# Kernel tuning notes

Measured on AMD Instinct MI355X. Metric: run time of the kernel, lower is better.

Reference implementation:

```python
import jax, jax.numpy as jnp
import numpy as np

NUM_JOINTS = 50
FEAT = 3 * NUM_JOINTS  # 150

def _skeleton_bones():
    # Standard 50-joint sign-language skeleton (body + two 21-joint hands).
    body = [(0, 1), (1, 2), (2, 3), (3, 4), (1, 5), (5, 6), (6, 7)]
    def hand(conn_from, wrist):
        bones = [(conn_from, wrist)]
        for f in range(5):  # 5 fingers, chains of 4 joints from the wrist
            base = wrist + 1 + 4 * f
            bones.append((wrist, base))
            for k in range(3):
                bones.append((base + k, base + k + 1))
        return bones
    bones = body + hand(7, 8) + hand(4, 29)  # 49 bones
    bones.append((0, 2))  # pad to 50 bones so 3*num_bones == 150 matches the mask
    return np.asarray(bones, dtype=np.int32)

_BONES = _skeleton_bones()
_BA = jnp.asarray(_BONES[:, 0])  # (50,) bone endpoint a
_BB = jnp.asarray(_BONES[:, 1])  # (50,) bone endpoint b

def get_length_direct(x):
    # x: (B, T, 150) -> lengths (B, T, 50), directs (B, T, 150)
    B, T, _ = x.shape
    joints = x.reshape(B, T, NUM_JOINTS, 3)
    diff = joints[:, :, _BA, :] - joints[:, :, _BB, :]  # (B, T, 50, 3)
    length = jnp.sqrt(jnp.sum(diff * diff, axis=-1, keepdims=True))  # (B, T, 50, 1)
    tiny = jnp.finfo(x.dtype).tiny
    direct = diff / (length + tiny)  # unit directions
    return length[..., 0], direct.reshape(B, T, -1)

def setup_inputs() -> dict:
    key = jax.random.key(0)
    k1, k2 = jax.random.split(key)
    B, T = 64, 4096
    preds = jax.random.normal(k1, (B, T, FEAT), dtype=jnp.float32)
    targets = jax.random.normal(k2, (B, T, FEAT), dtype=jnp.float32)
    return {"preds": preds, "targets": targets}

def reference(preds, targets):
    target_pad = 0.0
    m = (targets != target_pad).astype(preds.dtype)  # (B, T, 150)
    pm = preds * m
    tm = targets * m
    _, pd = get_length_direct(pm)   # (B, T, 150)
    _, td = get_length_direct(tm)
    pd = pd * m  # mask[:, :, :150] == full mask since 3*num_bones == 150
    td = td * m
    # criterion = L1 (mean), criterion_bone = MSE (mean)
    recon = jnp.mean(jnp.abs(pm - tm)) + 0.1 * jnp.mean((pd - td) ** 2)
    return recon
```

## Files before the change

kernel.cpp:

```cpp
#include <hip/hip_runtime.h>
#include <stdint.h>

#define NUM_BONES  50
#define FEAT       150
#define FPT        8
#define THREADS    256
#define TILE_FLOATS (FPT * FEAT)
#define TOTAL_FRAMES (64 * 4096)
#define TOTAL_TILES  (TOTAL_FRAMES / FPT)
#define GRID_BLOCKS  2048
#define TILES_PER_BLOCK (TOTAL_TILES / GRID_BLOCKS)
#define NTASK      (FPT * NUM_BONES)

__device__ __constant__ int c_ba[NUM_BONES] = {
    0, 1, 2, 3, 1, 5, 6,
    7, 8, 9, 10, 11, 8, 13, 14, 15, 8, 17, 18, 19,
    8, 21, 22, 23, 8, 25, 26, 27,
    4, 29, 30, 31, 32, 29, 34, 35, 36, 29, 38, 39, 40,
    29, 42, 43, 44, 29, 46, 47, 48,
    0
};
__device__ __constant__ int c_bb[NUM_BONES] = {
    1, 2, 3, 4, 5, 6, 7,
    8, 9, 10, 11, 12, 13, 14, 15, 16, 17, 18, 19, 20,
    21, 22, 23, 24, 25, 26, 27, 28,
    29, 30, 31, 32, 33, 34, 35, 36, 37, 38, 39, 40, 41,
    42, 43, 44, 45, 46, 47, 48, 49,
    2
};

#define AS1 __attribute__((address_space(1)))
#define AS3 __attribute__((address_space(3)))

__device__ __forceinline__ void gload16(const float* g, float* l)
{
    __builtin_amdgcn_global_load_lds((AS1 unsigned int*)(uintptr_t)g,
                                     (AS3 unsigned int*)(uintptr_t)l,
                                     16, 0, 0);
}

__device__ __forceinline__ void stage_tile(const float* __restrict__ src,
                                           float* lds, int wv, int ln, int tile)
{
    const float* base = src + (size_t)tile * TILE_FLOATS;
    gload16(base + ((wv * 64 + ln) << 2), lds + wv * 256);
    if (ln < 11)
        gload16(base + ((256 + wv * 11 + ln) << 2), lds + 1024 + wv * 44);
}

__device__ __forceinline__ void bone_task(const float* __restrict__ P,
                                          const float* __restrict__ T,
                                          int ja, int jb, int ob,
                                          float& l1, float& mse)
{
    float pax = P[ja], pay = P[ja + 1], paz = P[ja + 2];
    float pbx = P[jb], pby = P[jb + 1], pbz = P[jb + 2];
    float tax = T[ja], tay = T[ja + 1], taz = T[ja + 2];
    float tbx = T[jb], tby = T[jb + 1], tbz = T[jb + 2];
    float pox = P[ob], poy = P[ob + 1], poz = P[ob + 2];
    float tox = T[ob], toy = T[ob + 1], toz = T[ob + 2];

    pax = (tax != 0.0f) ? pax : 0.0f;
    pay = (tay != 0.0f) ? pay : 0.0f;
    paz = (taz != 0.0f) ? paz : 0.0f;
    pbx = (tbx != 0.0f) ? pbx : 0.0f;
    pby = (tby != 0.0f) ? pby : 0.0f;
    pbz = (tbz != 0.0f) ? pbz : 0.0f;
    pox = (tox != 0.0f) ? pox : 0.0f;
    poy = (toy != 0.0f) ? poy : 0.0f;
    poz = (toz != 0.0f) ? poz : 0.0f;

    l1 += fabsf(pox - tox) + fabsf(poy - toy) + fabsf(poz - toz);

    float dpx = pax - pbx, dpy = pay - pby, dpz = paz - pbz;
    float dtx = tax - tbx, dty = tay - tby, dtz = taz - tbz;
    float lp2 = dpx * dpx + dpy * dpy + dpz * dpz;
    float lt2 = dtx * dtx + dty * dty + dtz * dtz;
    float ip = (lp2 > 0.0f) ? __builtin_amdgcn_rsqf(lp2) : 0.0f;
    float it = (lt2 > 0.0f) ? __builtin_amdgcn_rsqf(lt2) : 0.0f;
    float e0 = dpx * ip - dtx * it;
    float e1 = dpy * ip - dty * it;
    float e2 = dpz * ip - dtz * it;
    mse += (tox != 0.0f) ? e0 * e0 : 0.0f;
    mse += (toy != 0.0f) ? e1 * e1 : 0.0f;
    mse += (toz != 0.0f) ? e2 * e2 : 0.0f;
}

__global__ __launch_bounds__(THREADS)
void loss_main(const float* __restrict__ preds,
               const float* __restrict__ targets,
               double* __restrict__ part0,
               double* __restrict__ part1)
{
    __shared__ float s_p[2][TILE_FLOATS];
    __shared__ float s_t[2][TILE_FLOATS];

    const int tid = threadIdx.x;
    const int wv = tid >> 6;
    const int ln = tid & 63;

    int ja0, jb0, ob0, ja1, jb1, ob1;
    {
        int f = tid & 7, b = tid >> 3;
        ja0 = f * FEAT + 3 * c_ba[b];
        jb0 = f * FEAT + 3 * c_bb[b];
        ob0 = f * FEAT + 3 * b;
        int i1 = tid + THREADS;
        int ii = (i1 < NTASK) ? i1 : 0;
        f = ii & 7; b = ii >> 3;
        ja1 = f * FEAT + 3 * c_ba[b];
        jb1 = f * FEAT + 3 * c_bb[b];
        ob1 = f * FEAT + 3 * b;
    }

    float l1 = 0.0f, mse = 0.0f;

    stage_tile(preds,   s_p[0], wv, ln, (int)blockIdx.x);
    stage_tile(targets, s_t[0], wv, ln, (int)blockIdx.x);

#pragma unroll 1
    for (int j = 0; j < TILES_PER_BLOCK; ++j) {
        const int bs = j & 1;
        if (j + 1 < TILES_PER_BLOCK) {
            const int tn = (int)blockIdx.x + (j + 1) * GRID_BLOCKS;
            stage_tile(preds,   s_p[bs ^ 1], wv, ln, tn);
            stage_tile(targets, s_t[bs ^ 1], wv, ln, tn);
            asm volatile("s_waitcnt vmcnt(4)" ::: "memory");
        } else {
            asm volatile("s_waitcnt vmcnt(0)" ::: "memory");
        }
        __builtin_amdgcn_sched_barrier(0);
        __builtin_amdgcn_s_barrier();
        __builtin_amdgcn_sched_barrier(0);

        const float* P = s_p[bs];
        const float* T = s_t[bs];
        bone_task(P, T, ja0, jb0, ob0, l1, mse);
        if (tid < (NTASK - THREADS))
            bone_task(P, T, ja1, jb1, ob1, l1, mse);

        __builtin_amdgcn_sched_barrier(0);
        __builtin_amdgcn_s_barrier();
    }

    double v0 = (double)l1;
    double v1 = (double)mse;
    for (int off = 32; off > 0; off >>= 1) {
        v0 += __shfl_down(v0, off, 64);
        v1 += __shfl_down(v1, off, 64);
    }
    __shared__ double s_red0[THREADS / 64];
    __shared__ double s_red1[THREADS / 64];
    if (ln == 0) { s_red0[wv] = v0; s_red1[wv] = v1; }
    __syncthreads();
    if (tid == 0) {
        part0[blockIdx.x] = s_red0[0] + s_red0[1] + s_red0[2] + s_red0[3];
        part1[blockIdx.x] = s_red1[0] + s_red1[1] + s_red1[2] + s_red1[3];
    }
}

__global__ __launch_bounds__(THREADS)
void loss_final(const double* __restrict__ part0,
                const double* __restrict__ part1,
                float* __restrict__ out)
{
    const int tid = threadIdx.x;
    double a = 0.0, b = 0.0;
    for (int i = tid; i < GRID_BLOCKS; i += THREADS) {
        a += part0[i];
        b += part1[i];
    }
    for (int off = 32; off > 0; off >>= 1) {
        a += __shfl_down(a, off, 64);
        b += __shfl_down(b, off, 64);
    }
    __shared__ double s0[THREADS / 64];
    __shared__ double s1[THREADS / 64];
    const int wave = tid >> 6;
    const int lane = tid & 63;
    if (lane == 0) { s0[wave] = a; s1[wave] = b; }
    __syncthreads();
    if (tid == 0) {
        double sa = s0[0] + s0[1] + s0[2] + s0[3];
        double sb = s1[0] + s1[1] + s1[2] + s1[3];
        const double N = 64.0 * 4096.0 * 150.0;
        out[0] = (float)(sa / N + 0.1 * (sb / N));
    }
}

extern "C" void kernel_launch(void* const* d_in, const int* in_sizes, int n_in,
                              void* d_out, int out_size, void* d_ws, size_t ws_size,
                              hipStream_t stream)
{
    (void)in_sizes; (void)n_in; (void)out_size; (void)ws_size;
    const float* preds   = (const float*)d_in[0];
    const float* targets = (const float*)d_in[1];
    double* part0 = (double*)d_ws;
    double* part1 = part0 + GRID_BLOCKS;

    loss_main<<<GRID_BLOCKS, THREADS, 0, stream>>>(preds, targets, part0, part1);
    loss_final<<<1, THREADS, 0, stream>>>(part0, part1, (float*)d_out);
}
```

Baseline: 325.1 us.

## Give each wave its own 4-deep LDS ring of 2-frame tiles, drop block barriers

Before, all four waves of a block shared one 8-frame tile with double buffering and two block barriers per tile. Now each wave owns a private 4-slot LDS ring of 2-frame tiles, prefetched three tiles ahead with vmcnt waits, and walks a contiguous range of tiles. The grid shrinks to 1024 blocks. The aim is to remove block-wide synchronisation and keep more loads in flight. In exchange each tile is smaller and lane utilisation is lower (100 bone tasks over 128 lane slots), and the waitcnt constants depend on the exact load count per stage.

After: 327.4 us. About the same (+0.7%).

```diff
diff --git a/kernel.cpp b/kernel.cpp
--- a/kernel.cpp
+++ b/kernel.cpp
@@ -3,14 +3,17 @@
 
 #define NUM_BONES  50
 #define FEAT       150
-#define FPT        8
+#define W          2
+#define TILE_F     (W * FEAT)
 #define THREADS    256
-#define TILE_FLOATS (FPT * FEAT)
+#define WPB        (THREADS / 64)
+#define GRID_BLOCKS 1024
+#define NWAVES     (GRID_BLOCKS * WPB)
 #define TOTAL_FRAMES (64 * 4096)
-#define TOTAL_TILES  (TOTAL_FRAMES / FPT)
-#define GRID_BLOCKS  2048
-#define TILES_PER_BLOCK (TOTAL_TILES / GRID_BLOCKS)
-#define NTASK      (FPT * NUM_BONES)
+#define TOTAL_TILES  (TOTAL_FRAMES / W)
+#define TPW        (TOTAL_TILES / NWAVES)
+#define DEPTH      4
+#define NTASK      (W * NUM_BONES)
 
 __device__ __constant__ int c_ba[NUM_BONES] = {
     0, 1, 2, 3, 1, 5, 6,
@@ -39,13 +42,19 @@
                                      16, 0, 0);
 }
 
-__device__ __forceinline__ void stage_tile(const float* __restrict__ src,
-                                           float* lds, int wv, int ln, int tile)
-{
-    const float* base = src + (size_t)tile * TILE_FLOATS;
-    gload16(base + ((wv * 64 + ln) << 2), lds + wv * 256);
-    if (ln < 11)
-        gload16(base + ((256 + wv * 11 + ln) << 2), lds + 1024 + wv * 44);
+__device__ __forceinline__ void stage_pair(const float* __restrict__ preds,
+                                           const float* __restrict__ targets,
+                                           float* slotP, float* slotT,
+                                           int ln, long long tile)
+{
+    const float* p = preds   + tile * TILE_F;
+    const float* t = targets + tile * TILE_F;
+    gload16(p + (ln << 2), slotP);
+    gload16(t + (ln << 2), slotT);
+    if (ln < 11) {
+        gload16(p + ((64 + ln) << 2), slotP + 256);
+        gload16(t + ((64 + ln) << 2), slotT + 256);
+    }
 }
 
 __device__ __forceinline__ void bone_task(const float* __restrict__ P,
@@ -92,55 +101,61 @@
                double* __restrict__ part0,
                double* __restrict__ part1)
 {
-    __shared__ float s_p[2][TILE_FLOATS];
-    __shared__ float s_t[2][TILE_FLOATS];
+    __shared__ float s_ring[WPB][DEPTH][2][TILE_F];
 
     const int tid = threadIdx.x;
     const int wv = tid >> 6;
     const int ln = tid & 63;
+    const long long wid = (long long)blockIdx.x * WPB + wv;
+    const long long tbase = wid * TPW;
 
     int ja0, jb0, ob0, ja1, jb1, ob1;
     {
-        int f = tid & 7, b = tid >> 3;
+        int b = ln >> 1, f = ln & 1;
         ja0 = f * FEAT + 3 * c_ba[b];
         jb0 = f * FEAT + 3 * c_bb[b];
         ob0 = f * FEAT + 3 * b;
-        int i1 = tid + THREADS;
+        int i1 = 64 + ln;
         int ii = (i1 < NTASK) ? i1 : 0;
-        f = ii & 7; b = ii >> 3;
+        b = ii >> 1; f = ii & 1;
         ja1 = f * FEAT + 3 * c_ba[b];
         jb1 = f * FEAT + 3 * c_bb[b];
         ob1 = f * FEAT + 3 * b;
     }
 
+    float* wbase = &s_ring[wv][0][0][0];
+
     float l1 = 0.0f, mse = 0.0f;
 
-    stage_tile(preds,   s_p[0], wv, ln, (int)blockIdx.x);
-    stage_tile(targets, s_t[0], wv, ln, (int)blockIdx.x);
+#pragma unroll
+    for (int s = 0; s < DEPTH - 1; ++s) {
+        float* sp = wbase + s * (2 * TILE_F);
+        stage_pair(preds, targets, sp, sp + TILE_F, ln, tbase + s);
+    }
 
 #pragma unroll 1
-    for (int j = 0; j < TILES_PER_BLOCK; ++j) {
-        const int bs = j & 1;
-        if (j + 1 < TILES_PER_BLOCK) {
-            const int tn = (int)blockIdx.x + (j + 1) * GRID_BLOCKS;
-            stage_tile(preds,   s_p[bs ^ 1], wv, ln, tn);
-            stage_tile(targets, s_t[bs ^ 1], wv, ln, tn);
-            asm volatile("s_waitcnt vmcnt(4)" ::: "memory");
+    for (int t = 0; t < TPW; ++t) {
+        const int slot = t & (DEPTH - 1);
+        if (t + DEPTH - 1 < TPW) {
+            const int ns = (t + DEPTH - 1) & (DEPTH - 1);
+            float* sp = wbase + ns * (2 * TILE_F);
+            stage_pair(preds, targets, sp, sp + TILE_F, ln,
+                       tbase + t + DEPTH - 1);
+            asm volatile("s_waitcnt vmcnt(12)" ::: "memory");
         } else {
-            asm volatile("s_waitcnt vmcnt(0)" ::: "memory");
+            const int rem = TPW - t;
+            if (rem == 3)      asm volatile("s_waitcnt vmcnt(8)" ::: "memory");
+            else if (rem == 2) asm volatile("s_waitcnt vmcnt(4)" ::: "memory");
+            else               asm volatile("s_waitcnt vmcnt(0)" ::: "memory");
         }
         __builtin_amdgcn_sched_barrier(0);
-        __builtin_amdgcn_s_barrier();
+
+        const float* P = wbase + slot * (2 * TILE_F);
+        const float* T = P + TILE_F;
+        bone_task(P, T, ja0, jb0, ob0, l1, mse);
+        if (ln < (NTASK - 64))
+            bone_task(P, T, ja1, jb1, ob1, l1, mse);
         __builtin_amdgcn_sched_barrier(0);
-
-        const float* P = s_p[bs];
-        const float* T = s_t[bs];
-        bone_task(P, T, ja0, jb0, ob0, l1, mse);
-        if (tid < (NTASK - THREADS))
-            bone_task(P, T, ja1, jb1, ob1, l1, mse);
-
-        __builtin_amdgcn_sched_barrier(0);
-        __builtin_amdgcn_s_barrier();
     }
 
     double v0 = (double)l1;
@@ -149,8 +164,8 @@
         v0 += __shfl_down(v0, off, 64);
         v1 += __shfl_down(v1, off, 64);
     }
-    __shared__ double s_red0[THREADS / 64];
-    __shared__ double s_red1[THREADS / 64];
+    __shared__ double s_red0[WPB];
+    __shared__ double s_red1[WPB];
     if (ln == 0) { s_red0[wv] = v0; s_red1[wv] = v1; }
     __syncthreads();
     if (tid == 0) {
```
